# Optimization experiments

Hardware: AMD Instinct MI355X
Metric: run time of the kernel (lower is better)

## Reference

```python
import jax, jax.numpy as jnp
import numpy as np

N_NODES = 100000
N_EDGES = 1600000
IN_SIZE = 256
HIDDEN = 128
OUT_SIZE = 128


def setup_inputs() -> dict:
    key = jax.random.key(0)
    ks = jax.random.split(key, 8)
    X = jax.random.normal(ks[0], (N_NODES, IN_SIZE), dtype=jnp.float32)
    W1 = jax.random.normal(ks[1], (IN_SIZE, HIDDEN), dtype=jnp.float32) * (1.0 / np.sqrt(IN_SIZE))
    b1 = jax.random.normal(ks[2], (HIDDEN,), dtype=jnp.float32) * 0.01
    W2 = jax.random.normal(ks[3], (HIDDEN, OUT_SIZE), dtype=jnp.float32) * (1.0 / np.sqrt(HIDDEN))
    b2 = jax.random.normal(ks[4], (OUT_SIZE,), dtype=jnp.float32) * 0.01
    vals = jax.random.uniform(ks[5], (N_EDGES,), dtype=jnp.float32)
    row = jax.random.randint(ks[6], (N_EDGES,), 0, N_NODES, dtype=jnp.int64 if jax.config.jax_enable_x64 else jnp.int32)
    col = jax.random.randint(ks[7], (N_EDGES,), 0, N_NODES, dtype=jnp.int64 if jax.config.jax_enable_x64 else jnp.int32)
    return {"X": X, "W1": W1, "b1": b1, "W2": W2, "b2": b2,
            "vals": vals, "row": row, "col": col}


def _spmm(row, col, vals, H, n_nodes):
    # out[i] = sum_{e: row[e]==i} vals[e] * H[col[e]]  (COO SpMM)
    gathered = vals[:, None] * H[col]              # [E, d]
    return jax.ops.segment_sum(gathered, row, num_segments=n_nodes)


def reference(X, W1, b1, W2, b2, vals, row, col):
    n = X.shape[0]
    H = _spmm(row, col, vals, X @ W1 + b1, n)      # layer 1: Linear -> SpMM
    H = jax.nn.relu(H)
    out = _spmm(row, col, vals, H @ W2 + b2, n)    # layer 2: Linear -> SpMM
    return out
```

## Files before the change

kernel.cpp:

```cpp
#include <hip/hip_runtime.h>

#define N_NODES 100000
#define N_EDGES 1600000
#define NBINS 1563
#define CHUNK 8192
#define NBLK 196

typedef __attribute__((ext_vector_type(8))) short bf16x8;
typedef __attribute__((ext_vector_type(4))) float f32x4;

__device__ __forceinline__ unsigned int f2bf(float f) {
    unsigned int u = __float_as_uint(f);
    u += 0x7fffu + ((u >> 16) & 1u);
    return u >> 16;
}
__device__ __forceinline__ float bflo(unsigned int h) { return __uint_as_float(h << 16); }
__device__ __forceinline__ float bfhi(unsigned int h) { return __uint_as_float(h & 0xffff0000u); }

__global__ __launch_bounds__(256)
void conv_w(const float* __restrict__ W1, const float* __restrict__ W2,
            unsigned short* __restrict__ W1t, unsigned short* __restrict__ W2t)
{
    int idx = blockIdx.x * 256 + threadIdx.x;
    if (idx < 256 * 128) {
        int k = idx >> 7, n = idx & 127;
        W1t[(size_t)n * 256 + k] = (unsigned short)f2bf(W1[idx]);
    } else if (idx < 256 * 128 + 128 * 128) {
        int j = idx - 256 * 128;
        int k = j >> 7, n = j & 127;
        W2t[(size_t)n * 128 + k] = (unsigned short)f2bf(W2[j]);
    }
}

template<int K, bool ABF16>
__global__ __launch_bounds__(256, 3)
void gemm_mfma(const void* __restrict__ Av, const unsigned short* __restrict__ Wt,
               const float* __restrict__ bias, unsigned short* __restrict__ C, int M)
{
    constexpr int BK = 64;
    constexpr int PK = BK + 8;
    __shared__ unsigned short As[128 * PK];
    __shared__ unsigned short Bs[128 * PK];

    const int t    = threadIdx.x;
    const int m0   = blockIdx.x * 128;
    const int lane = t & 63;
    const int wv   = t >> 6;
    const int wm   = (wv >> 1) * 64;
    const int wn   = (wv & 1) * 64;
    const int l15  = lane & 15;
    const int quad = lane >> 4;

    f32x4 acc[4][4] = {};

    for (int k0 = 0; k0 < K; k0 += BK) {
        if (!ABF16) {
            const float* A = (const float*)Av;
            #pragma unroll
            for (int p = 0; p < 8; ++p) {
                int q  = p * 256 + t;
                int m  = q >> 4;
                int kq = (q & 15) << 2;
                int gm = m0 + m; if (gm >= M) gm = M - 1;
                float4 v = *(const float4*)(A + (size_t)gm * K + k0 + kq);
                unsigned int p0 = (f2bf(v.y) << 16) | f2bf(v.x);
                unsigned int p1 = (f2bf(v.w) << 16) | f2bf(v.z);
                *(uint2*)&As[m * PK + kq] = make_uint2(p0, p1);
            }
        } else {
            const unsigned short* A = (const unsigned short*)Av;
            #pragma unroll
            for (int p = 0; p < 4; ++p) {
                int q = p * 256 + t;
                int m = q >> 3;
                int g = q & 7;
                int gm = m0 + m; if (gm >= M) gm = M - 1;
                int4 v = *(const int4*)(A + (size_t)gm * K + k0 + g * 8);
                *(int4*)&As[m * PK + g * 8] = v;
            }
        }
        #pragma unroll
        for (int p = 0; p < 4; ++p) {
            int q = p * 256 + t;
            int n = q >> 3;
            int g = q & 7;
            int4 v = *(const int4*)(Wt + (size_t)n * K + k0 + g * 8);
            *(int4*)&Bs[n * PK + g * 8] = v;
        }
        __syncthreads();
        #pragma unroll
        for (int kk = 0; kk < BK; kk += 32) {
            bf16x8 a[4], b[4];
            #pragma unroll
            for (int i = 0; i < 4; ++i)
                a[i] = *(const bf16x8*)&As[(wm + i * 16 + l15) * PK + kk + quad * 8];
            #pragma unroll
            for (int j = 0; j < 4; ++j)
                b[j] = *(const bf16x8*)&Bs[(wn + j * 16 + l15) * PK + kk + quad * 8];
            #pragma unroll
            for (int i = 0; i < 4; ++i)
                #pragma unroll
                for (int j = 0; j < 4; ++j)
                    acc[i][j] = __builtin_amdgcn_mfma_f32_16x16x32_bf16(a[i], b[j], acc[i][j], 0, 0, 0);
        }
        __syncthreads();
    }

    float bv[4];
    #pragma unroll
    for (int j = 0; j < 4; ++j) bv[j] = bias[wn + j * 16 + l15];
    #pragma unroll
    for (int i = 0; i < 4; ++i) {
        #pragma unroll
        for (int r = 0; r < 4; ++r) {
            int gm = m0 + wm + i * 16 + quad * 4 + r;
            if (gm < M) {
                #pragma unroll
                for (int j = 0; j < 4; ++j)
                    C[(size_t)gm * 128 + wn + j * 16 + l15] =
                        (unsigned short)f2bf(acc[i][j][r] + bv[j]);
            }
        }
    }
}

__global__ __launch_bounds__(256)
void hist_block(const int* __restrict__ row, int* __restrict__ hist, int E)
{
    __shared__ int h[NBINS];
    const int t = threadIdx.x, b = blockIdx.x;
    for (int i = t; i < NBINS; i += 256) h[i] = 0;
    __syncthreads();
    const int s = b * CHUNK, e = min(E, s + CHUNK);
    for (int p = s + t; p < e; p += 256)
        atomicAdd(&h[row[p] >> 6], 1);
    __syncthreads();
    for (int i = t; i < NBINS; i += 256)
        hist[(size_t)b * NBINS + i] = h[i];
}

__global__ __launch_bounds__(256)
void scan_cols(int* __restrict__ hist, int* __restrict__ bincnt, int nblk)
{
    int bin  = (blockIdx.x * 256 + threadIdx.x) >> 6;
    int lane = threadIdx.x & 63;
    if (bin >= NBINS) return;
    int run = 0;
    for (int r0 = 0; r0 < nblk; r0 += 64) {
        int idx = r0 + lane;
        int v = (idx < nblk) ? hist[(size_t)idx * NBINS + bin] : 0;
        int incl = v;
        #pragma unroll
        for (int o = 1; o < 64; o <<= 1) {
            int u = __shfl_up(incl, o, 64);
            if (lane >= o) incl += u;
        }
        if (idx < nblk) hist[(size_t)idx * NBINS + bin] = run + incl - v;
        run += __shfl(incl, 63, 64);
    }
    if (lane == 0) bincnt[bin] = run;
}

__global__ __launch_bounds__(256)
void bin_scan(const int* __restrict__ bincnt, int* __restrict__ binptr,
              int* __restrict__ rowptr, int E)
{
    __shared__ int sd[256];
    const int PER = (NBINS + 255) / 256;
    int t = threadIdx.x;
    int v[PER]; int run = 0;
    #pragma unroll
    for (int j = 0; j < PER; ++j) {
        int idx = t * PER + j;
        int c = (idx < NBINS) ? bincnt[idx] : 0;
        v[j] = run; run += c;
    }
    sd[t] = run;
    __syncthreads();
    for (int off = 1; off < 256; off <<= 1) {
        int x = (t >= off) ? sd[t - off] : 0;
        __syncthreads();
        sd[t] += x;
        __syncthreads();
    }
    int toff = sd[t] - run;
    #pragma unroll
    for (int j = 0; j < PER; ++j) {
        int idx = t * PER + j;
        if (idx < NBINS) binptr[idx] = toff + v[j];
    }
    if (t == 255) { binptr[NBINS] = E; rowptr[N_NODES] = E; }
}

__global__ __launch_bounds__(256)
void scatter_bins(const int* __restrict__ row, const int* __restrict__ col,
                  const float* __restrict__ vals, const int* __restrict__ binptr,
                  const int* __restrict__ hist, int2* __restrict__ ep, int E)
{
    __shared__ int cur[NBINS];
    const int t = threadIdx.x, b = blockIdx.x;
    for (int i = t; i < NBINS; i += 256)
        cur[i] = binptr[i] + hist[(size_t)b * NBINS + i];
    __syncthreads();
    const int s = b * CHUNK, e = min(E, s + CHUNK);
    for (int p = s + t; p < e; p += 256) {
        int r = row[p];
        int pos = atomicAdd(&cur[r >> 6], 1);
        ep[pos] = make_int2(col[p] | ((r & 63) << 17), __float_as_int(vals[p]));
    }
}

__global__ __launch_bounds__(256)
void sort_bin(const int2* __restrict__ ep, int2* __restrict__ ep2,
              const int* __restrict__ binptr, int* __restrict__ rowptr, int n)
{
    __shared__ int cnt[64];
    __shared__ int cur[64];
    const int t   = threadIdx.x;
    const int bin = blockIdx.x;
    const int s = binptr[bin], e = binptr[bin + 1];

    if (t < 64) cnt[t] = 0;
    __syncthreads();
    for (int p = s + t; p < e; p += 256)
        atomicAdd(&cnt[(unsigned)ep[p].x >> 17], 1);
    __syncthreads();
    if (t < 64) {
        int c = cnt[t];
        int incl = c;
        #pragma unroll
        for (int o = 1; o < 64; o <<= 1) {
            int u = __shfl_up(incl, o, 64);
            if (t >= o) incl += u;
        }
        int base = s + incl - c;
        cur[t] = base;
        int gr = bin * 64 + t;
        if (gr < n) rowptr[gr] = base;
    }
    __syncthreads();
    for (int p = s + t; p < e; p += 256) {
        int2 m = ep[p];
        int pos = atomicAdd(&cur[(unsigned)m.x >> 17], 1);
        ep2[pos] = m;
    }
}

template<bool RELU, bool OUTBF16>
__global__ __launch_bounds__(256)
void spmm_csr(const int* __restrict__ rowptr, const int2* __restrict__ ep,
              const unsigned int* __restrict__ H, void* __restrict__ outv, int n)
{
    int wid  = (blockIdx.x * 256 + threadIdx.x) >> 6;
    int lane = threadIdx.x & 63;
    if (wid >= n) return;
    const int s = rowptr[wid], e = rowptr[wid + 1];

    float ax0 = 0.f, ay0 = 0.f, ax1 = 0.f, ay1 = 0.f;
    float ax2 = 0.f, ay2 = 0.f, ax3 = 0.f, ay3 = 0.f;

    for (int p = s; p < e; p += 8) {
        int2 m0 = ep[p],     m1 = ep[p + 1], m2 = ep[p + 2], m3 = ep[p + 3];
        int2 m4 = ep[p + 4], m5 = ep[p + 5], m6 = ep[p + 6], m7 = ep[p + 7];
        int c0 = m0.x & 0x1FFFF;
        int c1 = (p + 1 < e) ? (m1.x & 0x1FFFF) : 0;
        int c2 = (p + 2 < e) ? (m2.x & 0x1FFFF) : 0;
        int c3 = (p + 3 < e) ? (m3.x & 0x1FFFF) : 0;
        int c4 = (p + 4 < e) ? (m4.x & 0x1FFFF) : 0;
        int c5 = (p + 5 < e) ? (m5.x & 0x1FFFF) : 0;
        int c6 = (p + 6 < e) ? (m6.x & 0x1FFFF) : 0;
        int c7 = (p + 7 < e) ? (m7.x & 0x1FFFF) : 0;
        unsigned int h0 = H[(size_t)c0 * 64 + lane];
        unsigned int h1 = H[(size_t)c1 * 64 + lane];
        unsigned int h2 = H[(size_t)c2 * 64 + lane];
        unsigned int h3 = H[(size_t)c3 * 64 + lane];
        unsigned int h4 = H[(size_t)c4 * 64 + lane];
        unsigned int h5 = H[(size_t)c5 * 64 + lane];
        unsigned int h6 = H[(size_t)c6 * 64 + lane];
        unsigned int h7 = H[(size_t)c7 * 64 + lane];
        float v0 = __int_as_float(m0.y);
        float v1 = (p + 1 < e) ? __int_as_float(m1.y) : 0.f;
        float v2 = (p + 2 < e) ? __int_as_float(m2.y) : 0.f;
        float v3 = (p + 3 < e) ? __int_as_float(m3.y) : 0.f;
        float v4 = (p + 4 < e) ? __int_as_float(m4.y) : 0.f;
        float v5 = (p + 5 < e) ? __int_as_float(m5.y) : 0.f;
        float v6 = (p + 6 < e) ? __int_as_float(m6.y) : 0.f;
        float v7 = (p + 7 < e) ? __int_as_float(m7.y) : 0.f;
        ax0 = fmaf(v0, bflo(h0), ax0); ay0 = fmaf(v0, bfhi(h0), ay0);
        ax1 = fmaf(v1, bflo(h1), ax1); ay1 = fmaf(v1, bfhi(h1), ay1);
        ax2 = fmaf(v2, bflo(h2), ax2); ay2 = fmaf(v2, bfhi(h2), ay2);
        ax3 = fmaf(v3, bflo(h3), ax3); ay3 = fmaf(v3, bfhi(h3), ay3);
        ax0 = fmaf(v4, bflo(h4), ax0); ay0 = fmaf(v4, bfhi(h4), ay0);
        ax1 = fmaf(v5, bflo(h5), ax1); ay1 = fmaf(v5, bfhi(h5), ay1);
        ax2 = fmaf(v6, bflo(h6), ax2); ay2 = fmaf(v6, bfhi(h6), ay2);
        ax3 = fmaf(v7, bflo(h7), ax3); ay3 = fmaf(v7, bfhi(h7), ay3);
    }
    float ax = (ax0 + ax1) + (ax2 + ax3);
    float ay = (ay0 + ay1) + (ay2 + ay3);
    if (RELU) { ax = fmaxf(ax, 0.f); ay = fmaxf(ay, 0.f); }
    if (OUTBF16) {
        ((unsigned int*)outv)[(size_t)wid * 64 + lane] = (f2bf(ay) << 16) | f2bf(ax);
    } else {
        ((float2*)outv)[(size_t)wid * 64 + lane] = make_float2(ax, ay);
    }
}

extern "C" void kernel_launch(void* const* d_in, const int* in_sizes, int n_in,
                              void* d_out, int out_size, void* d_ws, size_t ws_size,
                              hipStream_t stream)
{
    const float* X    = (const float*)d_in[0];
    const float* W1   = (const float*)d_in[1];
    const float* b1   = (const float*)d_in[2];
    const float* W2   = (const float*)d_in[3];
    const float* b2   = (const float*)d_in[4];
    const float* vals = (const float*)d_in[5];
    const int*   row  = (const int*)d_in[6];
    const int*   col  = (const int*)d_in[7];
    float* out = (float*)d_out;

    char* ws = (char*)d_ws;
    size_t off = 0;
    auto alloc = [&](size_t bytes) -> void* {
        void* p = ws + off;
        off += (bytes + 511) & ~(size_t)511;
        return p;
    };
    unsigned short* Y1     = (unsigned short*)alloc((size_t)N_NODES * 128 * 2);
    unsigned short* Hbuf   = (unsigned short*)alloc((size_t)N_NODES * 128 * 2);
    int2*           ep     = (int2*) alloc((size_t)(N_EDGES + 8) * 8);
    int2*           ep2    = (int2*) alloc((size_t)(N_EDGES + 8) * 8);
    int*            hist   = (int*)  alloc((size_t)NBLK * NBINS * 4);
    int*            bincnt = (int*)  alloc((size_t)NBINS * 4);
    int*            binptr = (int*)  alloc((size_t)(NBINS + 1) * 4);
    int*            rowptr = (int*)  alloc((size_t)(N_NODES + 1) * 4);
    unsigned short* W1t    = (unsigned short*)alloc((size_t)128 * 256 * 2);
    unsigned short* W2t    = (unsigned short*)alloc((size_t)128 * 128 * 2);

    conv_w<<<(256 * 128 + 128 * 128 + 255) / 256, 256, 0, stream>>>(W1, W2, W1t, W2t);

    hipMemsetAsync(ep2 + N_EDGES, 0, 8 * sizeof(int2), stream);
    hist_block<<<NBLK, 256, 0, stream>>>(row, hist, N_EDGES);
    scan_cols<<<(NBINS * 64 + 255) / 256, 256, 0, stream>>>(hist, bincnt, NBLK);
    bin_scan<<<1, 256, 0, stream>>>(bincnt, binptr, rowptr, N_EDGES);
    scatter_bins<<<NBLK, 256, 0, stream>>>(row, col, vals, binptr, hist, ep, N_EDGES);
    sort_bin<<<NBINS, 256, 0, stream>>>(ep, ep2, binptr, rowptr, N_NODES);

    const int gblocks = (N_NODES + 127) / 128;
    gemm_mfma<256, false><<<gblocks, 256, 0, stream>>>(X, W1t, b1, Y1, N_NODES);
    spmm_csr<true, true><<<(N_NODES + 3) / 4, 256, 0, stream>>>(rowptr, ep2, (const unsigned int*)Y1, Hbuf, N_NODES);

    gemm_mfma<128, true><<<gblocks, 256, 0, stream>>>(Hbuf, W2t, b2, Y1, N_NODES);
    spmm_csr<false, false><<<(N_NODES + 3) / 4, 256, 0, stream>>>(rowptr, ep2, (const unsigned int*)Y1, out, N_NODES);
}
```

Measured before the change: 436.6 us.

## Split wavefront into four edge groups with 16-byte row gathers in SpMM

The CSR SpMM kernel now divides each 64-lane wavefront into four 16-lane groups. Each group handles a different edge and gathers a full 256-byte bf16 row with uint4 loads, instead of all lanes reading 4-byte pieces of one edge's row. Partial sums are combined across groups with xor shuffles, and half the lanes write the result with vector stores. This aims to cut the number of memory instructions and process more edges in parallel, at the cost of shuffle reductions, wasted lanes when a row has few edges, and extra padding in the edge buffer.

```diff
diff --git a/kernel.cpp b/kernel.cpp
--- a/kernel.cpp
+++ b/kernel.cpp
@@ -255,53 +255,82 @@
     int lane = threadIdx.x & 63;
     if (wid >= n) return;
     const int s = rowptr[wid], e = rowptr[wid + 1];
-
-    float ax0 = 0.f, ay0 = 0.f, ax1 = 0.f, ay1 = 0.f;
-    float ax2 = 0.f, ay2 = 0.f, ax3 = 0.f, ay3 = 0.f;
-
-    for (int p = s; p < e; p += 8) {
-        int2 m0 = ep[p],     m1 = ep[p + 1], m2 = ep[p + 2], m3 = ep[p + 3];
-        int2 m4 = ep[p + 4], m5 = ep[p + 5], m6 = ep[p + 6], m7 = ep[p + 7];
-        int c0 = m0.x & 0x1FFFF;
-        int c1 = (p + 1 < e) ? (m1.x & 0x1FFFF) : 0;
-        int c2 = (p + 2 < e) ? (m2.x & 0x1FFFF) : 0;
-        int c3 = (p + 3 < e) ? (m3.x & 0x1FFFF) : 0;
-        int c4 = (p + 4 < e) ? (m4.x & 0x1FFFF) : 0;
-        int c5 = (p + 5 < e) ? (m5.x & 0x1FFFF) : 0;
-        int c6 = (p + 6 < e) ? (m6.x & 0x1FFFF) : 0;
-        int c7 = (p + 7 < e) ? (m7.x & 0x1FFFF) : 0;
-        unsigned int h0 = H[(size_t)c0 * 64 + lane];
-        unsigned int h1 = H[(size_t)c1 * 64 + lane];
-        unsigned int h2 = H[(size_t)c2 * 64 + lane];
-        unsigned int h3 = H[(size_t)c3 * 64 + lane];
-        unsigned int h4 = H[(size_t)c4 * 64 + lane];
-        unsigned int h5 = H[(size_t)c5 * 64 + lane];
-        unsigned int h6 = H[(size_t)c6 * 64 + lane];
-        unsigned int h7 = H[(size_t)c7 * 64 + lane];
-        float v0 = __int_as_float(m0.y);
-        float v1 = (p + 1 < e) ? __int_as_float(m1.y) : 0.f;
-        float v2 = (p + 2 < e) ? __int_as_float(m2.y) : 0.f;
-        float v3 = (p + 3 < e) ? __int_as_float(m3.y) : 0.f;
-        float v4 = (p + 4 < e) ? __int_as_float(m4.y) : 0.f;
-        float v5 = (p + 5 < e) ? __int_as_float(m5.y) : 0.f;
-        float v6 = (p + 6 < e) ? __int_as_float(m6.y) : 0.f;
-        float v7 = (p + 7 < e) ? __int_as_float(m7.y) : 0.f;
-        ax0 = fmaf(v0, bflo(h0), ax0); ay0 = fmaf(v0, bfhi(h0), ay0);
-        ax1 = fmaf(v1, bflo(h1), ax1); ay1 = fmaf(v1, bfhi(h1), ay1);
-        ax2 = fmaf(v2, bflo(h2), ax2); ay2 = fmaf(v2, bfhi(h2), ay2);
-        ax3 = fmaf(v3, bflo(h3), ax3); ay3 = fmaf(v3, bfhi(h3), ay3);
-        ax0 = fmaf(v4, bflo(h4), ax0); ay0 = fmaf(v4, bfhi(h4), ay0);
-        ax1 = fmaf(v5, bflo(h5), ax1); ay1 = fmaf(v5, bfhi(h5), ay1);
-        ax2 = fmaf(v6, bflo(h6), ax2); ay2 = fmaf(v6, bfhi(h6), ay2);
-        ax3 = fmaf(v7, bflo(h7), ax3); ay3 = fmaf(v7, bfhi(h7), ay3);
-    }
-    float ax = (ax0 + ax1) + (ax2 + ax3);
-    float ay = (ay0 + ay1) + (ay2 + ay3);
-    if (RELU) { ax = fmaxf(ax, 0.f); ay = fmaxf(ay, 0.f); }
+    const int quad = lane >> 4;
+    const int s16  = lane & 15;
+    const uint4* __restrict__ H4 = (const uint4*)H;
+
+    float a0 = 0.f, a1 = 0.f, a2 = 0.f, a3 = 0.f;
+    float a4 = 0.f, a5 = 0.f, a6 = 0.f, a7 = 0.f;
+
+    for (int p = s; p < e; p += 16) {
+        int e0 = p + quad, e1 = p + 4 + quad, e2 = p + 8 + quad, e3 = p + 12 + quad;
+        int2 m0 = ep[e0];
+        int2 m1 = ep[e1];
+        int2 m2 = ep[e2];
+        int2 m3 = ep[e3];
+        int c0 = (e0 < e) ? (m0.x & 0x1FFFF) : 0;
+        int c1 = (e1 < e) ? (m1.x & 0x1FFFF) : 0;
+        int c2 = (e2 < e) ? (m2.x & 0x1FFFF) : 0;
+        int c3 = (e3 < e) ? (m3.x & 0x1FFFF) : 0;
+        uint4 h0 = H4[(size_t)(c0 * 16 + s16)];
+        uint4 h1 = H4[(size_t)(c1 * 16 + s16)];
+        uint4 h2 = H4[(size_t)(c2 * 16 + s16)];
+        uint4 h3 = H4[(size_t)(c3 * 16 + s16)];
+        float v0 = (e0 < e) ? __int_as_float(m0.y) : 0.f;
+        float v1 = (e1 < e) ? __int_as_float(m1.y) : 0.f;
+        float v2 = (e2 < e) ? __int_as_float(m2.y) : 0.f;
+        float v3 = (e3 < e) ? __int_as_float(m3.y) : 0.f;
+        a0 = fmaf(v0, bflo(h0.x), a0); a1 = fmaf(v0, bfhi(h0.x), a1);
+        a2 = fmaf(v0, bflo(h0.y), a2); a3 = fmaf(v0, bfhi(h0.y), a3);
+        a4 = fmaf(v0, bflo(h0.z), a4); a5 = fmaf(v0, bfhi(h0.z), a5);
+        a6 = fmaf(v0, bflo(h0.w), a6); a7 = fmaf(v0, bfhi(h0.w), a7);
+        a0 = fmaf(v1, bflo(h1.x), a0); a1 = fmaf(v1, bfhi(h1.x), a1);
+        a2 = fmaf(v1, bflo(h1.y), a2); a3 = fmaf(v1, bfhi(h1.y), a3);
+        a4 = fmaf(v1, bflo(h1.z), a4); a5 = fmaf(v1, bfhi(h1.z), a5);
+        a6 = fmaf(v1, bflo(h1.w), a6); a7 = fmaf(v1, bfhi(h1.w), a7);
+        a0 = fmaf(v2, bflo(h2.x), a0); a1 = fmaf(v2, bfhi(h2.x), a1);
+        a2 = fmaf(v2, bflo(h2.y), a2); a3 = fmaf(v2, bfhi(h2.y), a3);
+        a4 = fmaf(v2, bflo(h2.z), a4); a5 = fmaf(v2, bfhi(h2.z), a5);
+        a6 = fmaf(v2, bflo(h2.w), a6); a7 = fmaf(v2, bfhi(h2.w), a7);
+        a0 = fmaf(v3, bflo(h3.x), a0); a1 = fmaf(v3, bfhi(h3.x), a1);
+        a2 = fmaf(v3, bflo(h3.y), a2); a3 = fmaf(v3, bfhi(h3.y), a3);
+        a4 = fmaf(v3, bflo(h3.z), a4); a5 = fmaf(v3, bfhi(h3.z), a5);
+        a6 = fmaf(v3, bflo(h3.w), a6); a7 = fmaf(v3, bfhi(h3.w), a7);
+    }
+
+    a0 += __shfl_xor(a0, 16, 64); a0 += __shfl_xor(a0, 32, 64);
+    a1 += __shfl_xor(a1, 16, 64); a1 += __shfl_xor(a1, 32, 64);
+    a2 += __shfl_xor(a2, 16, 64); a2 += __shfl_xor(a2, 32, 64);
+    a3 += __shfl_xor(a3, 16, 64); a3 += __shfl_xor(a3, 32, 64);
+    a4 += __shfl_xor(a4, 16, 64); a4 += __shfl_xor(a4, 32, 64);
+    a5 += __shfl_xor(a5, 16, 64); a5 += __shfl_xor(a5, 32, 64);
+    a6 += __shfl_xor(a6, 16, 64); a6 += __shfl_xor(a6, 32, 64);
+    a7 += __shfl_xor(a7, 16, 64); a7 += __shfl_xor(a7, 32, 64);
+
+    if (RELU) {
+        a0 = fmaxf(a0, 0.f); a1 = fmaxf(a1, 0.f); a2 = fmaxf(a2, 0.f); a3 = fmaxf(a3, 0.f);
+        a4 = fmaxf(a4, 0.f); a5 = fmaxf(a5, 0.f); a6 = fmaxf(a6, 0.f); a7 = fmaxf(a7, 0.f);
+    }
+
     if (OUTBF16) {
-        ((unsigned int*)outv)[(size_t)wid * 64 + lane] = (f2bf(ay) << 16) | f2bf(ax);
+        if (quad < 2) {
+            unsigned int w0, w1;
+            if (quad == 0) {
+                w0 = (f2bf(a1) << 16) | f2bf(a0);
+                w1 = (f2bf(a3) << 16) | f2bf(a2);
+            } else {
+                w0 = (f2bf(a5) << 16) | f2bf(a4);
+                w1 = (f2bf(a7) << 16) | f2bf(a6);
+            }
+            *(uint2*)((unsigned int*)outv + (size_t)wid * 64 + s16 * 4 + quad * 2) =
+                make_uint2(w0, w1);
+        }
     } else {
-        ((float2*)outv)[(size_t)wid * 64 + lane] = make_float2(ax, ay);
+        if (quad < 2) {
+            float4 w = (quad == 0) ? make_float4(a0, a1, a2, a3)
+                                   : make_float4(a4, a5, a6, a7);
+            *(float4*)((float*)outv + (size_t)wid * 128 + s16 * 8 + quad * 4) = w;
+        }
     }
 }
 
@@ -328,8 +357,8 @@
     };
     unsigned short* Y1     = (unsigned short*)alloc((size_t)N_NODES * 128 * 2);
     unsigned short* Hbuf   = (unsigned short*)alloc((size_t)N_NODES * 128 * 2);
-    int2*           ep     = (int2*) alloc((size_t)(N_EDGES + 8) * 8);
-    int2*           ep2    = (int2*) alloc((size_t)(N_EDGES + 8) * 8);
+    int2*           ep     = (int2*) alloc((size_t)(N_EDGES + 16) * 8);
+    int2*           ep2    = (int2*) alloc((size_t)(N_EDGES + 16) * 8);
     int*            hist   = (int*)  alloc((size_t)NBLK * NBINS * 4);
     int*            bincnt = (int*)  alloc((size_t)NBINS * 4);
     int*            binptr = (int*)  alloc((size_t)(NBINS + 1) * 4);
@@ -339,7 +368,7 @@
 
     conv_w<<<(256 * 128 + 128 * 128 + 255) / 256, 256, 0, stream>>>(W1, W2, W1t, W2t);
 
-    hipMemsetAsync(ep2 + N_EDGES, 0, 8 * sizeof(int2), stream);
+    hipMemsetAsync(ep2 + N_EDGES, 0, 16 * sizeof(int2), stream);
     hist_block<<<NBLK, 256, 0, stream>>>(row, hist, N_EDGES);
     scan_cols<<<(NBINS * 64 + 255) / 256, 256, 0, stream>>>(hist, bincnt, NBLK);
     bin_scan<<<1, 256, 0, stream>>>(bincnt, binptr, rowptr, N_EDGES);
```

After: 412.4 us. -5.6%, faster.

## Split features into halves and compress edges for cache-friendly SpMM

Applied to the files above, without the earlier changes.

The GEMM now writes its 128-wide output as two 64-wide halves, and each SpMM layer runs twice, once per half. This shrinks the gathered feature working set so it fits better in L2 and last-level cache. Edges are packed into 4 bytes: a 17-bit column index plus the value as an fp16. The SpMM kernel is rewritten so that each group of 8 lanes processes one edge with 16-byte loads, followed by a shuffle reduction. The histogram chunk size is also halved and bf16 packing uses a cheaper perm-based rounding. In exchange it adds extra kernel launches and reduces the precision of the edge values.

```diff
diff --git a/kernel.cpp b/kernel.cpp
--- a/kernel.cpp
+++ b/kernel.cpp
@@ -1,10 +1,11 @@
 #include <hip/hip_runtime.h>
+#include <hip/hip_fp16.h>
 
 #define N_NODES 100000
 #define N_EDGES 1600000
 #define NBINS 1563
-#define CHUNK 8192
-#define NBLK 196
+#define CHUNK 4096
+#define NBLK 391
 
 typedef __attribute__((ext_vector_type(8))) short bf16x8;
 typedef __attribute__((ext_vector_type(4))) float f32x4;
@@ -16,6 +17,12 @@
 }
 __device__ __forceinline__ float bflo(unsigned int h) { return __uint_as_float(h << 16); }
 __device__ __forceinline__ float bfhi(unsigned int h) { return __uint_as_float(h & 0xffff0000u); }
+
+__device__ __forceinline__ unsigned int pack2bf(float x, float y) {
+    unsigned int ux = __float_as_uint(x) + 0x8000u;
+    unsigned int uy = __float_as_uint(y) + 0x8000u;
+    return __builtin_amdgcn_perm(uy, ux, 0x07060302u);
+}
 
 __global__ __launch_bounds__(256)
 void conv_w(const float* __restrict__ W1, const float* __restrict__ W2,
@@ -34,8 +41,9 @@
 
 template<int K, bool ABF16>
 __global__ __launch_bounds__(256, 3)
-void gemm_mfma(const void* __restrict__ Av, const unsigned short* __restrict__ Wt,
-               const float* __restrict__ bias, unsigned short* __restrict__ C, int M)
+void gemm_mfma(const void* __restrict__ Av, const void* __restrict__ Avh,
+               const unsigned short* __restrict__ Wt, const float* __restrict__ bias,
+               unsigned short* __restrict__ Clo, unsigned short* __restrict__ Chi, int M)
 {
     constexpr int BK = 64;
     constexpr int PK = BK + 8;
@@ -63,19 +71,20 @@
                 int kq = (q & 15) << 2;
                 int gm = m0 + m; if (gm >= M) gm = M - 1;
                 float4 v = *(const float4*)(A + (size_t)gm * K + k0 + kq);
-                unsigned int p0 = (f2bf(v.y) << 16) | f2bf(v.x);
-                unsigned int p1 = (f2bf(v.w) << 16) | f2bf(v.z);
+                unsigned int p0 = pack2bf(v.x, v.y);
+                unsigned int p1 = pack2bf(v.z, v.w);
                 *(uint2*)&As[m * PK + kq] = make_uint2(p0, p1);
             }
         } else {
-            const unsigned short* A = (const unsigned short*)Av;
+            const unsigned short* Asrc = (k0 == 0) ? (const unsigned short*)Av
+                                                   : (const unsigned short*)Avh;
             #pragma unroll
             for (int p = 0; p < 4; ++p) {
                 int q = p * 256 + t;
                 int m = q >> 3;
                 int g = q & 7;
                 int gm = m0 + m; if (gm >= M) gm = M - 1;
-                int4 v = *(const int4*)(A + (size_t)gm * K + k0 + g * 8);
+                int4 v = *(const int4*)(Asrc + (size_t)gm * 64 + g * 8);
                 *(int4*)&As[m * PK + g * 8] = v;
             }
         }
@@ -109,6 +118,7 @@
     float bv[4];
     #pragma unroll
     for (int j = 0; j < 4; ++j) bv[j] = bias[wn + j * 16 + l15];
+    unsigned short* Cw = wn ? Chi : Clo;
     #pragma unroll
     for (int i = 0; i < 4; ++i) {
         #pragma unroll
@@ -117,7 +127,7 @@
             if (gm < M) {
                 #pragma unroll
                 for (int j = 0; j < 4; ++j)
-                    C[(size_t)gm * 128 + wn + j * 16 + l15] =
+                    Cw[(size_t)gm * 64 + j * 16 + l15] =
                         (unsigned short)f2bf(acc[i][j][r] + bv[j]);
             }
         }
@@ -211,7 +221,7 @@
 }
 
 __global__ __launch_bounds__(256)
-void sort_bin(const int2* __restrict__ ep, int2* __restrict__ ep2,
+void sort_bin(const int2* __restrict__ ep, unsigned int* __restrict__ ep2,
               const int* __restrict__ binptr, int* __restrict__ rowptr, int n)
 {
     __shared__ int cnt[64];
@@ -242,66 +252,77 @@
     for (int p = s + t; p < e; p += 256) {
         int2 m = ep[p];
         int pos = atomicAdd(&cur[(unsigned)m.x >> 17], 1);
-        ep2[pos] = m;
+        unsigned int v16 = __half_as_ushort(__float2half(__int_as_float(m.y)));
+        ep2[pos] = ((unsigned)m.x & 0x1FFFFu) | (v16 << 17);
     }
 }
 
 template<bool RELU, bool OUTBF16>
-__global__ __launch_bounds__(256)
-void spmm_csr(const int* __restrict__ rowptr, const int2* __restrict__ ep,
-              const unsigned int* __restrict__ H, void* __restrict__ outv, int n)
+__global__ __launch_bounds__(256, 8)
+void spmm_half(const int* __restrict__ rowptr, const unsigned int* __restrict__ ep,
+               const unsigned int* __restrict__ H, void* __restrict__ outv, int n)
 {
     int wid  = (blockIdx.x * 256 + threadIdx.x) >> 6;
     int lane = threadIdx.x & 63;
     if (wid >= n) return;
     const int s = rowptr[wid], e = rowptr[wid + 1];
-
-    float ax0 = 0.f, ay0 = 0.f, ax1 = 0.f, ay1 = 0.f;
-    float ax2 = 0.f, ay2 = 0.f, ax3 = 0.f, ay3 = 0.f;
-
-    for (int p = s; p < e; p += 8) {
-        int2 m0 = ep[p],     m1 = ep[p + 1], m2 = ep[p + 2], m3 = ep[p + 3];
-        int2 m4 = ep[p + 4], m5 = ep[p + 5], m6 = ep[p + 6], m7 = ep[p + 7];
-        int c0 = m0.x & 0x1FFFF;
-        int c1 = (p + 1 < e) ? (m1.x & 0x1FFFF) : 0;
-        int c2 = (p + 2 < e) ? (m2.x & 0x1FFFF) : 0;
-        int c3 = (p + 3 < e) ? (m3.x & 0x1FFFF) : 0;
-        int c4 = (p + 4 < e) ? (m4.x & 0x1FFFF) : 0;
-        int c5 = (p + 5 < e) ? (m5.x & 0x1FFFF) : 0;
-        int c6 = (p + 6 < e) ? (m6.x & 0x1FFFF) : 0;
-        int c7 = (p + 7 < e) ? (m7.x & 0x1FFFF) : 0;
-        unsigned int h0 = H[(size_t)c0 * 64 + lane];
-        unsigned int h1 = H[(size_t)c1 * 64 + lane];
-        unsigned int h2 = H[(size_t)c2 * 64 + lane];
-        unsigned int h3 = H[(size_t)c3 * 64 + lane];
-        unsigned int h4 = H[(size_t)c4 * 64 + lane];
-        unsigned int h5 = H[(size_t)c5 * 64 + lane];
-        unsigned int h6 = H[(size_t)c6 * 64 + lane];
-        unsigned int h7 = H[(size_t)c7 * 64 + lane];
-        float v0 = __int_as_float(m0.y);
-        float v1 = (p + 1 < e) ? __int_as_float(m1.y) : 0.f;
-        float v2 = (p + 2 < e) ? __int_as_float(m2.y) : 0.f;
-        float v3 = (p + 3 < e) ? __int_as_float(m3.y) : 0.f;
-        float v4 = (p + 4 < e) ? __int_as_float(m4.y) : 0.f;
-        float v5 = (p + 5 < e) ? __int_as_float(m5.y) : 0.f;
-        float v6 = (p + 6 < e) ? __int_as_float(m6.y) : 0.f;
-        float v7 = (p + 7 < e) ? __int_as_float(m7.y) : 0.f;
-        ax0 = fmaf(v0, bflo(h0), ax0); ay0 = fmaf(v0, bfhi(h0), ay0);
-        ax1 = fmaf(v1, bflo(h1), ax1); ay1 = fmaf(v1, bfhi(h1), ay1);
-        ax2 = fmaf(v2, bflo(h2), ax2); ay2 = fmaf(v2, bfhi(h2), ay2);
-        ax3 = fmaf(v3, bflo(h3), ax3); ay3 = fmaf(v3, bfhi(h3), ay3);
-        ax0 = fmaf(v4, bflo(h4), ax0); ay0 = fmaf(v4, bfhi(h4), ay0);
-        ax1 = fmaf(v5, bflo(h5), ax1); ay1 = fmaf(v5, bfhi(h5), ay1);
-        ax2 = fmaf(v6, bflo(h6), ax2); ay2 = fmaf(v6, bfhi(h6), ay2);
-        ax3 = fmaf(v7, bflo(h7), ax3); ay3 = fmaf(v7, bfhi(h7), ay3);
-    }
-    float ax = (ax0 + ax1) + (ax2 + ax3);
-    float ay = (ay0 + ay1) + (ay2 + ay3);
-    if (RELU) { ax = fmaxf(ax, 0.f); ay = fmaxf(ay, 0.f); }
-    if (OUTBF16) {
-        ((unsigned int*)outv)[(size_t)wid * 64 + lane] = (f2bf(ay) << 16) | f2bf(ax);
-    } else {
-        ((float2*)outv)[(size_t)wid * 64 + lane] = make_float2(ax, ay);
+    const int oct = lane >> 3;
+    const int s8  = lane & 7;
+    const uint4* __restrict__ H4 = (const uint4*)H;
+
+    float a0 = 0.f, a1 = 0.f, a2 = 0.f, a3 = 0.f;
+    float a4 = 0.f, a5 = 0.f, a6 = 0.f, a7 = 0.f;
+
+    int p = s;
+    for (; p + 8 <= e; p += 8) {
+        unsigned int pk = __builtin_nontemporal_load(&ep[p + oct]);
+        int c = pk & 0x1FFFF;
+        uint4 h = H4[(size_t)c * 8 + s8];
+        float v = __half2float(__ushort_as_half((unsigned short)(pk >> 17)));
+        a0 = fmaf(v, bflo(h.x), a0); a1 = fmaf(v, bfhi(h.x), a1);
+        a2 = fmaf(v, bflo(h.y), a2); a3 = fmaf(v, bfhi(h.y), a3);
+        a4 = fmaf(v, bflo(h.z), a4); a5 = fmaf(v, bfhi(h.z), a5);
+        a6 = fmaf(v, bflo(h.w), a6); a7 = fmaf(v, bfhi(h.w), a7);
+    }
+    if (p < e) {
+        int idx = p + oct;
+        unsigned int pk = __builtin_nontemporal_load(&ep[idx]);
+        int c = (idx < e) ? (int)(pk & 0x1FFFF) : 0;
+        uint4 h = H4[(size_t)c * 8 + s8];
+        float v = (idx < e) ? __half2float(__ushort_as_half((unsigned short)(pk >> 17))) : 0.f;
+        a0 = fmaf(v, bflo(h.x), a0); a1 = fmaf(v, bfhi(h.x), a1);
+        a2 = fmaf(v, bflo(h.y), a2); a3 = fmaf(v, bfhi(h.y), a3);
+        a4 = fmaf(v, bflo(h.z), a4); a5 = fmaf(v, bfhi(h.z), a5);
+        a6 = fmaf(v, bflo(h.w), a6); a7 = fmaf(v, bfhi(h.w), a7);
+    }
+
+    a0 += __shfl_xor(a0, 8, 64); a0 += __shfl_xor(a0, 16, 64); a0 += __shfl_xor(a0, 32, 64);
+    a1 += __shfl_xor(a1, 8, 64); a1 += __shfl_xor(a1, 16, 64); a1 += __shfl_xor(a1, 32, 64);
+    a2 += __shfl_xor(a2, 8, 64); a2 += __shfl_xor(a2, 16, 64); a2 += __shfl_xor(a2, 32, 64);
+    a3 += __shfl_xor(a3, 8, 64); a3 += __shfl_xor(a3, 16, 64); a3 += __shfl_xor(a3, 32, 64);
+    a4 += __shfl_xor(a4, 8, 64); a4 += __shfl_xor(a4, 16, 64); a4 += __shfl_xor(a4, 32, 64);
+    a5 += __shfl_xor(a5, 8, 64); a5 += __shfl_xor(a5, 16, 64); a5 += __shfl_xor(a5, 32, 64);
+    a6 += __shfl_xor(a6, 8, 64); a6 += __shfl_xor(a6, 16, 64); a6 += __shfl_xor(a6, 32, 64);
+    a7 += __shfl_xor(a7, 8, 64); a7 += __shfl_xor(a7, 16, 64); a7 += __shfl_xor(a7, 32, 64);
+
+    if (RELU) {
+        a0 = fmaxf(a0, 0.f); a1 = fmaxf(a1, 0.f); a2 = fmaxf(a2, 0.f); a3 = fmaxf(a3, 0.f);
+        a4 = fmaxf(a4, 0.f); a5 = fmaxf(a5, 0.f); a6 = fmaxf(a6, 0.f); a7 = fmaxf(a7, 0.f);
+    }
+
+    if (oct == 0) {
+        if (OUTBF16) {
+            uint4 w;
+            w.x = pack2bf(a0, a1); w.y = pack2bf(a2, a3);
+            w.z = pack2bf(a4, a5); w.w = pack2bf(a6, a7);
+            ((uint4*)outv)[(size_t)wid * 8 + s8] = w;
+        } else {
+            float* o = (float*)outv + (size_t)wid * 128 + s8 * 8;
+            f32x4 w0; w0[0] = a0; w0[1] = a1; w0[2] = a2; w0[3] = a3;
+            f32x4 w1; w1[0] = a4; w1[1] = a5; w1[2] = a6; w1[3] = a7;
+            __builtin_nontemporal_store(w0, (f32x4*)o);
+            __builtin_nontemporal_store(w1, (f32x4*)(o + 4));
+        }
     }
 }
 
@@ -326,10 +347,12 @@
         off += (bytes + 511) & ~(size_t)511;
         return p;
     };
-    unsigned short* Y1     = (unsigned short*)alloc((size_t)N_NODES * 128 * 2);
-    unsigned short* Hbuf   = (unsigned short*)alloc((size_t)N_NODES * 128 * 2);
+    unsigned short* Ylo    = (unsigned short*)alloc((size_t)N_NODES * 64 * 2);
+    unsigned short* Yhi    = (unsigned short*)alloc((size_t)N_NODES * 64 * 2);
+    unsigned short* Hlo    = (unsigned short*)alloc((size_t)N_NODES * 64 * 2);
+    unsigned short* Hhi    = (unsigned short*)alloc((size_t)N_NODES * 64 * 2);
     int2*           ep     = (int2*) alloc((size_t)(N_EDGES + 8) * 8);
-    int2*           ep2    = (int2*) alloc((size_t)(N_EDGES + 8) * 8);
+    unsigned int*   ep2    = (unsigned int*)alloc((size_t)(N_EDGES + 8) * 4);
     int*            hist   = (int*)  alloc((size_t)NBLK * NBINS * 4);
     int*            bincnt = (int*)  alloc((size_t)NBINS * 4);
     int*            binptr = (int*)  alloc((size_t)(NBINS + 1) * 4);
@@ -339,7 +362,8 @@
 
     conv_w<<<(256 * 128 + 128 * 128 + 255) / 256, 256, 0, stream>>>(W1, W2, W1t, W2t);
 
-    hipMemsetAsync(ep2 + N_EDGES, 0, 8 * sizeof(int2), stream);
+    hipError_t _e = hipMemsetAsync(ep2 + N_EDGES, 0, 8 * 4, stream);
+    (void)_e;
     hist_block<<<NBLK, 256, 0, stream>>>(row, hist, N_EDGES);
     scan_cols<<<(NBINS * 64 + 255) / 256, 256, 0, stream>>>(hist, bincnt, NBLK);
     bin_scan<<<1, 256, 0, stream>>>(bincnt, binptr, rowptr, N_EDGES);
@@ -347,9 +371,13 @@
     sort_bin<<<NBINS, 256, 0, stream>>>(ep, ep2, binptr, rowptr, N_NODES);
 
     const int gblocks = (N_NODES + 127) / 128;
-    gemm_mfma<256, false><<<gblocks, 256, 0, stream>>>(X, W1t, b1, Y1, N_NODES);
-    spmm_csr<true, true><<<(N_NODES + 3) / 4, 256, 0, stream>>>(rowptr, ep2, (const unsigned int*)Y1, Hbuf, N_NODES);
-
-    gemm_mfma<128, true><<<gblocks, 256, 0, stream>>>(Hbuf, W2t, b2, Y1, N_NODES);
-    spmm_csr<false, false><<<(N_NODES + 3) / 4, 256, 0, stream>>>(rowptr, ep2, (const unsigned int*)Y1, out, N_NODES);
-}
+    const int sblocks = (N_NODES + 3) / 4;
+
+    gemm_mfma<256, false><<<gblocks, 256, 0, stream>>>(X, nullptr, W1t, b1, Ylo, Yhi, N_NODES);
+    spmm_half<true, true><<<sblocks, 256, 0, stream>>>(rowptr, ep2, (const unsigned int*)Ylo, Hlo, N_NODES);
+    spmm_half<true, true><<<sblocks, 256, 0, stream>>>(rowptr, ep2, (const unsigned int*)Yhi, Hhi, N_NODES);
+
+    gemm_mfma<128, true><<<gblocks, 256, 0, stream>>>(Hlo, Hhi, W2t, b2, Ylo, Yhi, N_NODES);
+    spmm_half<false, false><<<sblocks, 256, 0, stream>>>(rowptr, ep2, (const unsigned int*)Ylo, out, N_NODES);
+    spmm_half<false, false><<<sblocks, 256, 0, stream>>>(rowptr, ep2, (const unsigned int*)Yhi, out + 64, N_NODES);
+}
```

Measured after the change: 478.2 us. 1.1x slower.
